# Optimization experiments

Measured on AMD Instinct MI355X. Metric: run time of the kernel, lower is better.

## Reference

```python
import jax, jax.numpy as jnp
import numpy as np

B, T, H, L, NB, NL = 32, 512, 256, 2048, 256, 4
F0_MIN, F0_MAX = 0.0, 1.0
E_MIN, E_MAX = 0.0, 1.0


def setup_inputs() -> dict:
    key = jax.random.key(0)
    ks = jax.random.split(key, 12)
    s = 1.0 / np.sqrt(H)
    return {
        "x": jax.random.normal(ks[0], (B, T, H), jnp.float32),
        "src_seq": jax.random.uniform(ks[1], (B, T, 3), jnp.float32, 1.0, 8.0),
        "duration_target": jax.random.randint(ks[2], (B, T), 0, 7, jnp.int32),
        "pitch_target": jax.random.uniform(ks[3], (B, L), jnp.float32),
        "energy_target": jax.random.uniform(ks[4], (B, L), jnp.float32),
        "src_mask": jnp.zeros((B, T), bool),
        "max_len": L,
        "dur_W": jax.random.normal(ks[5], (NL, H, H), jnp.float32) * s,
        "dur_b": jnp.zeros((NL, H), jnp.float32),
        "dur_w": jax.random.normal(ks[6], (H,), jnp.float32) * s,
        "dur_b2": jnp.zeros((1,), jnp.float32),
        "pit_W": jax.random.normal(ks[7], (NL, H, H), jnp.float32) * s,
        "pit_b": jnp.zeros((NL, H), jnp.float32),
        "pit_w": jax.random.normal(ks[8], (H,), jnp.float32) * s,
        "pit_b2": jnp.zeros((1,), jnp.float32),
        "en_W": jax.random.normal(ks[9], (NL, H, H), jnp.float32) * s,
        "en_b": jnp.zeros((NL, H), jnp.float32),
        "en_w": jax.random.normal(ks[10], (H,), jnp.float32) * s,
        "en_b2": jnp.zeros((1,), jnp.float32),
        "pitch_emb": jax.random.normal(ks[11], (2 * NB, H), jnp.float32),
        "energy_emb": jax.random.normal(jax.random.fold_in(key, 99), (2 * NB, H), jnp.float32),
    }


def _predictor(h, W, b, w, b2, mask):
    # stand-in for Decoder(n_layers=4) + Linear(H, 1) head
    for i in range(NL):
        h = jax.nn.relu(jnp.einsum('blh,hk->blk', h, W[i]) + b[i])
    out = jnp.einsum('blh,h->bl', h, w) + b2[0]
    return jnp.where(mask, 0.0, out)


def _length_regulate(x, dur, max_len):
    # cumsum-based repeat_interleave: frame m maps to token searchsorted(cumsum(dur), m, 'right')
    cum = jnp.cumsum(dur, axis=1)                      # [B, T]
    mel_len = jnp.minimum(cum[:, -1], max_len)         # [B]
    frames = jnp.arange(max_len)                       # [L]
    idx = jax.vmap(lambda c: jnp.searchsorted(c, frames, side='right'))(cum)
    idx = jnp.clip(idx, 0, x.shape[1] - 1)             # [B, L]
    out = jnp.take_along_axis(x, idx[:, :, None], axis=1)  # [B, L, H]
    mel_mask = frames[None, :] >= mel_len[:, None]     # True = padding
    out = out * (~mel_mask)[:, :, None]
    return out, mel_len, mel_mask


def reference(x, src_seq, duration_target, pitch_target, energy_target, src_mask, max_len,
              dur_W, dur_b, dur_w, dur_b2, pit_W, pit_b, pit_w, pit_b2,
              en_W, en_b, en_w, en_b2, pitch_emb, energy_emb):
    # duration predictor: LengthPredictor = decoder + linear + tanh, scaled by note lengths
    d = _predictor(x, dur_W, dur_b, dur_w, dur_b2, src_mask)
    log_duration_prediction = (jnp.tanh(d) + 1.0) * src_seq[:, :, 2]

    # length regulator (training path: duration_target provided)
    xe, mel_len, mel_mask = _length_regulate(x, duration_target, max_len)

    pitch_prediction = jax.nn.relu(_predictor(xe, pit_W, pit_b, pit_w, pit_b2, mel_mask))
    p_idx = jnp.ceil((pitch_target - F0_MIN) / (F0_MAX - F0_MIN) * NB).astype(jnp.int32)
    p_emb = pitch_emb[p_idx]                            # [B, L, H]

    energy_prediction = _predictor(xe, en_W, en_b, en_w, en_b2, mel_mask)
    e_idx = jnp.ceil((energy_target - E_MIN) / (E_MAX - E_MIN) * NB).astype(jnp.int32)
    e_emb = energy_emb[e_idx]                           # [B, L, H]

    out = xe + p_emb + e_emb
    return out, log_duration_prediction, pitch_prediction, energy_prediction, mel_len, mel_mask
```

## Files before the change

kernel.cpp:

```cpp
#include <hip/hip_runtime.h>

typedef _Float16 half_t;
typedef _Float16 half8 __attribute__((ext_vector_type(8)));
typedef float floatx4 __attribute__((ext_vector_type(4)));

#define HST 264
#define B_ 32
#define T_ 512
#define H_ 256
#define L_ 2048

__global__ void prep_weights_kernel(const float* __restrict__ dur_W,
                                    const float* __restrict__ pit_W,
                                    const float* __restrict__ en_W,
                                    half_t* __restrict__ Wp) {
  int g = blockIdx.x * 256 + threadIdx.x;
  int lane = g & 63;
  int t = g >> 6;
  int nt = t & 15;
  int kk = (t >> 4) & 7;
  int layer = (t >> 7) & 3;
  int pred = t >> 9;
  const float* W = (pred == 0 ? dur_W : (pred == 1 ? pit_W : en_W)) + layer * 65536;
  int n = nt * 16 + (lane & 15);
  int k0 = kk * 32 + (lane >> 4) * 8;
  half8 o;
#pragma unroll
  for (int j = 0; j < 8; ++j) o[j] = (half_t)W[(k0 + j) * 256 + n];
  *(half8*)&Wp[(size_t)t * 512 + lane * 8] = o;
}

__global__ void regulate_kernel(const float* __restrict__ x,
                                const int* __restrict__ dur,
                                const float* __restrict__ pitch_t,
                                const float* __restrict__ energy_t,
                                const float* __restrict__ pemb,
                                const float* __restrict__ eemb,
                                int* __restrict__ idx_ws,
                                int* __restrict__ ml_ws,
                                float* __restrict__ out0,
                                float* __restrict__ out4,
                                float* __restrict__ out5) {
  __shared__ int cum_l[T_];
  __shared__ int idx_l[128];
  __shared__ int ml_s;
  int tid = threadIdx.x;
  int b = blockIdx.x >> 4;
  int chunk = blockIdx.x & 15;

  if (tid < 64) {
    int l = tid;
    const int* dr = dur + b * T_;
    int v[8];
    int base = l * 8;
#pragma unroll
    for (int j = 0; j < 8; ++j) v[j] = dr[base + j];
#pragma unroll
    for (int j = 1; j < 8; ++j) v[j] += v[j - 1];
    int tot = v[7];
    int inc = tot;
    for (int d = 1; d < 64; d <<= 1) {
      int t = __shfl_up(inc, d);
      if (l >= d) inc += t;
    }
    int excl = inc - tot;
#pragma unroll
    for (int j = 0; j < 8; ++j) cum_l[base + j] = excl + v[j];
    if (l == 63) {
      int mel = min(inc, L_);
      ml_s = mel;
      if (chunk == 0) {
        ml_ws[b] = mel;
        out4[b] = (float)mel;
      }
    }
  }
  __syncthreads();
  int ml = ml_s;
  if (tid < 128) {
    int m = chunk * 128 + tid;
    int lo = 0;
#pragma unroll
    for (int sh = 8; sh >= 0; --sh) {
      int c = lo + (1 << sh);
      if (c <= T_ && cum_l[c - 1] <= m) lo = c;
    }
    int idx = min(lo, T_ - 1);
    idx_l[tid] = idx;
    int g = b * L_ + m;
    idx_ws[g] = idx;
    out5[g] = (m >= ml) ? 1.0f : 0.0f;
  }
  __syncthreads();
  int wv = tid >> 6, lane = tid & 63;
  for (int it = 0; it < 32; ++it) {
    int p = wv * 32 + it;
    int m = chunk * 128 + p;
    int g = b * L_ + m;
    int ir = idx_l[p];
    float xv0 = 0.f, xv1 = 0.f, xv2 = 0.f, xv3 = 0.f;
    if (m < ml) {
      const float4 xv = *(const float4*)&x[((size_t)(b * T_ + ir)) * H_ + lane * 4];
      xv0 = xv.x; xv1 = xv.y; xv2 = xv.z; xv3 = xv.w;
    }
    int pi = (int)ceilf(pitch_t[g] * 256.0f);
    int ei = (int)ceilf(energy_t[g] * 256.0f);
    const float4 pv = *(const float4*)&pemb[(size_t)pi * H_ + lane * 4];
    const float4 ev = *(const float4*)&eemb[(size_t)ei * H_ + lane * 4];
    float4 o;
    o.x = xv0 + pv.x + ev.x;
    o.y = xv1 + pv.y + ev.y;
    o.z = xv2 + pv.z + ev.z;
    o.w = xv3 + pv.w + ev.w;
    *(float4*)&out0[(size_t)g * H_ + lane * 4] = o;
  }
}

__global__ __launch_bounds__(256, 2) void predictor_kernel(
    const float* __restrict__ x,
    const half_t* __restrict__ Wp,
    const float* __restrict__ dur_b, const float* __restrict__ dur_w, const float* __restrict__ dur_b2,
    const float* __restrict__ pit_b, const float* __restrict__ pit_w, const float* __restrict__ pit_b2,
    const float* __restrict__ en_b,  const float* __restrict__ en_w,  const float* __restrict__ en_b2,
    const int* __restrict__ idx_ws, const int* __restrict__ mlw,
    const float* __restrict__ src_seq, const unsigned char* __restrict__ src_mask,
    float* __restrict__ out1, float* __restrict__ out2, float* __restrict__ out3) {
  __shared__ half_t hlds[128 * HST];
  int bid = blockIdx.x;
  int mode, blk;
  const half_t* W; const float* bias; const float* wh; const float* b2p; float* outp;
  if (bid < 512)       { mode = 1; blk = bid;        W = Wp + 262144; bias = pit_b; wh = pit_w; b2p = pit_b2; outp = out2; }
  else if (bid < 1024) { mode = 2; blk = bid - 512;  W = Wp + 524288; bias = en_b;  wh = en_w;  b2p = en_b2;  outp = out3; }
  else                 { mode = 0; blk = bid - 1024; W = Wp;          bias = dur_b; wh = dur_w; b2p = dur_b2; outp = out1; }

  int tid = threadIdx.x;
  int wv = tid >> 6, lane = tid & 63;
  int mi = lane & 15, qi = lane >> 4;
  int wrow0 = wv * 32;
  int brow0 = blk * 128;

  if (mode == 0) {
    for (int it = 0; it < 32; ++it) {
      int row = brow0 + wrow0 + it;
      const float4 xv = *(const float4*)&x[(size_t)row * H_ + lane * 4];
      half_t* dst = &hlds[(wrow0 + it) * HST + lane * 4];
      dst[0] = (half_t)xv.x; dst[1] = (half_t)xv.y;
      dst[2] = (half_t)xv.z; dst[3] = (half_t)xv.w;
    }
  } else {
    int b = brow0 >> 11;
    int m0 = brow0 & (L_ - 1);
    int ml = mlw[b];
    for (int it = 0; it < 32; ++it) {
      int m = m0 + wrow0 + it;
      float x0 = 0.f, x1 = 0.f, x2 = 0.f, x3 = 0.f;
      if (m < ml) {
        int ir = idx_ws[b * L_ + m];
        const float4 xv = *(const float4*)&x[((size_t)(b * T_ + ir)) * H_ + lane * 4];
        x0 = xv.x; x1 = xv.y; x2 = xv.z; x3 = xv.w;
      }
      half_t* dst = &hlds[(wrow0 + it) * HST + lane * 4];
      dst[0] = (half_t)x0; dst[1] = (half_t)x1;
      dst[2] = (half_t)x2; dst[3] = (half_t)x3;
    }
  }

  for (int layer = 0; layer < 4; ++layer) {
    half8 afr0[8], afr1[8];
#pragma unroll
    for (int kk = 0; kk < 8; ++kk) {
      afr0[kk] = *(const half8*)&hlds[(wrow0 + mi) * HST + kk * 32 + qi * 8];
      afr1[kk] = *(const half8*)&hlds[(wrow0 + 16 + mi) * HST + kk * 32 + qi * 8];
    }
    const half_t* wl = W + (size_t)layer * 65536;
    const float* bl = bias + layer * 256;
    half8 bA[8], bB[8];
#pragma unroll
    for (int kk = 0; kk < 8; ++kk)
      bA[kk] = *(const half8*)&wl[(size_t)(kk * 16 + 0) * 512 + lane * 8];
#pragma unroll 1
    for (int nt2 = 0; nt2 < 8; ++nt2) {
      int nt0 = nt2 * 2;
#pragma unroll
      for (int kk = 0; kk < 8; ++kk)
        bB[kk] = *(const half8*)&wl[(size_t)(kk * 16 + nt0 + 1) * 512 + lane * 8];
      {
        float bn = bl[nt0 * 16 + mi];
        floatx4 acc0 = {bn, bn, bn, bn};
        floatx4 acc1 = {bn, bn, bn, bn};
#pragma unroll
        for (int kk = 0; kk < 8; ++kk) {
          acc0 = __builtin_amdgcn_mfma_f32_16x16x32_f16(afr0[kk], bA[kk], acc0, 0, 0, 0);
          acc1 = __builtin_amdgcn_mfma_f32_16x16x32_f16(afr1[kk], bA[kk], acc1, 0, 0, 0);
        }
#pragma unroll
        for (int r = 0; r < 4; ++r) {
          float v0 = fmaxf(acc0[r], 0.f);
          float v1 = fmaxf(acc1[r], 0.f);
          hlds[(wrow0 + qi * 4 + r) * HST + nt0 * 16 + mi] = (half_t)v0;
          hlds[(wrow0 + 16 + qi * 4 + r) * HST + nt0 * 16 + mi] = (half_t)v1;
        }
      }
      if (nt2 < 7) {
#pragma unroll
        for (int kk = 0; kk < 8; ++kk)
          bA[kk] = *(const half8*)&wl[(size_t)(kk * 16 + nt0 + 2) * 512 + lane * 8];
      }
      {
        float bn = bl[(nt0 + 1) * 16 + mi];
        floatx4 acc0 = {bn, bn, bn, bn};
        floatx4 acc1 = {bn, bn, bn, bn};
#pragma unroll
        for (int kk = 0; kk < 8; ++kk) {
          acc0 = __builtin_amdgcn_mfma_f32_16x16x32_f16(afr0[kk], bB[kk], acc0, 0, 0, 0);
          acc1 = __builtin_amdgcn_mfma_f32_16x16x32_f16(afr1[kk], bB[kk], acc1, 0, 0, 0);
        }
#pragma unroll
        for (int r = 0; r < 4; ++r) {
          float v0 = fmaxf(acc0[r], 0.f);
          float v1 = fmaxf(acc1[r], 0.f);
          hlds[(wrow0 + qi * 4 + r) * HST + (nt0 + 1) * 16 + mi] = (half_t)v0;
          hlds[(wrow0 + 16 + qi * 4 + r) * HST + (nt0 + 1) * 16 + mi] = (half_t)v1;
        }
      }
    }
  }

  {
    int r = lane >> 1, hf = lane & 1;
    int lrow = wrow0 + r;
    float sum = 0.f;
    const half_t* hrow = &hlds[lrow * HST + hf * 128];
    const float* whp = wh + hf * 128;
#pragma unroll
    for (int j = 0; j < 16; ++j) {
      half8 hv = *(const half8*)&hrow[j * 8];
#pragma unroll
      for (int u = 0; u < 8; ++u) sum += (float)hv[u] * whp[j * 8 + u];
    }
    sum += __shfl_xor(sum, 1);
    if (hf == 0) {
      int row = brow0 + lrow;
      float d = sum + b2p[0];
      if (mode == 0) {
        if (src_mask[row]) d = 0.f;
        float s2 = src_seq[(size_t)row * 3 + 2];
        outp[row] = (tanhf(d) + 1.0f) * s2;
      } else {
        int b = row >> 11;
        int m = row & (L_ - 1);
        float v = (m >= mlw[b]) ? 0.f : d;
        outp[row] = (mode == 1) ? fmaxf(v, 0.f) : v;
      }
    }
  }
}

extern "C" void kernel_launch(void* const* d_in, const int* in_sizes, int n_in,
                              void* d_out, int out_size, void* d_ws, size_t ws_size,
                              hipStream_t stream) {
  const float* x        = (const float*)d_in[0];
  const float* src_seq  = (const float*)d_in[1];
  const int*   durt     = (const int*)d_in[2];
  const float* pitcht   = (const float*)d_in[3];
  const float* energyt  = (const float*)d_in[4];
  const unsigned char* src_mask = (const unsigned char*)d_in[5];
  const float* dur_W  = (const float*)d_in[7];
  const float* dur_b  = (const float*)d_in[8];
  const float* dur_w  = (const float*)d_in[9];
  const float* dur_b2 = (const float*)d_in[10];
  const float* pit_W  = (const float*)d_in[11];
  const float* pit_b  = (const float*)d_in[12];
  const float* pit_w  = (const float*)d_in[13];
  const float* pit_b2 = (const float*)d_in[14];
  const float* en_W   = (const float*)d_in[15];
  const float* en_b   = (const float*)d_in[16];
  const float* en_w   = (const float*)d_in[17];
  const float* en_b2  = (const float*)d_in[18];
  const float* pemb   = (const float*)d_in[19];
  const float* eemb   = (const float*)d_in[20];

  float* out0 = (float*)d_out;
  float* out1 = out0 + 16777216;
  float* out2 = out1 + 16384;
  float* out3 = out2 + 65536;
  float* out4 = out3 + 65536;
  float* out5 = out4 + 32;

  int* idx_ws = (int*)d_ws;
  int* ml_ws  = idx_ws + 65536;
  half_t* Wp  = (half_t*)((char*)d_ws + 262272);

  prep_weights_kernel<<<dim3(384), dim3(256), 0, stream>>>(dur_W, pit_W, en_W, Wp);
  regulate_kernel<<<dim3(512), dim3(256), 0, stream>>>(x, durt, pitcht, energyt, pemb, eemb,
                                                       idx_ws, ml_ws, out0, out4, out5);
  predictor_kernel<<<dim3(1152), dim3(256), 0, stream>>>(
      x, Wp,
      dur_b, dur_w, dur_b2,
      pit_b, pit_w, pit_b2,
      en_b, en_w, en_b2,
      idx_ws, ml_ws, src_seq, src_mask,
      out1, out2, out3);
}
```

Measured before the change: 282.7 us.

## Split regulate into meta and out0 kernels; restructure predictor to 2-wave column-split MFMA

```diff
diff --git a/kernel.cpp b/kernel.cpp
--- a/kernel.cpp
+++ b/kernel.cpp
@@ -1,6 +1,7 @@
 #include <hip/hip_runtime.h>
 
 typedef _Float16 half_t;
+typedef _Float16 half4 __attribute__((ext_vector_type(4)));
 typedef _Float16 half8 __attribute__((ext_vector_type(8)));
 typedef float floatx4 __attribute__((ext_vector_type(4)));
 
@@ -30,24 +31,19 @@
   *(half8*)&Wp[(size_t)t * 512 + lane * 8] = o;
 }
 
-__global__ void regulate_kernel(const float* __restrict__ x,
-                                const int* __restrict__ dur,
-                                const float* __restrict__ pitch_t,
-                                const float* __restrict__ energy_t,
-                                const float* __restrict__ pemb,
-                                const float* __restrict__ eemb,
-                                int* __restrict__ idx_ws,
-                                int* __restrict__ ml_ws,
-                                float* __restrict__ out0,
-                                float* __restrict__ out4,
-                                float* __restrict__ out5) {
+__global__ void meta_kernel(const int* __restrict__ dur,
+                            const float* __restrict__ pitch_t,
+                            const float* __restrict__ energy_t,
+                            int* __restrict__ idx_ws,
+                            int* __restrict__ pi_ws,
+                            int* __restrict__ ei_ws,
+                            int* __restrict__ ml_ws,
+                            float* __restrict__ out4,
+                            float* __restrict__ out5) {
   __shared__ int cum_l[T_];
-  __shared__ int idx_l[128];
   __shared__ int ml_s;
+  int b = blockIdx.x;
   int tid = threadIdx.x;
-  int b = blockIdx.x >> 4;
-  int chunk = blockIdx.x & 15;
-
   if (tid < 64) {
     int l = tid;
     const int* dr = dur + b * T_;
@@ -69,16 +65,15 @@
     if (l == 63) {
       int mel = min(inc, L_);
       ml_s = mel;
-      if (chunk == 0) {
-        ml_ws[b] = mel;
-        out4[b] = (float)mel;
-      }
+      ml_ws[b] = mel;
+      out4[b] = (float)mel;
     }
   }
   __syncthreads();
   int ml = ml_s;
-  if (tid < 128) {
-    int m = chunk * 128 + tid;
+#pragma unroll
+  for (int j = 0; j < 8; ++j) {
+    int m = j * 256 + tid;
     int lo = 0;
 #pragma unroll
     for (int sh = 8; sh >= 0; --sh) {
@@ -86,37 +81,43 @@
       if (c <= T_ && cum_l[c - 1] <= m) lo = c;
     }
     int idx = min(lo, T_ - 1);
-    idx_l[tid] = idx;
     int g = b * L_ + m;
     idx_ws[g] = idx;
+    pi_ws[g] = (int)ceilf(pitch_t[g] * 256.0f);
+    ei_ws[g] = (int)ceilf(energy_t[g] * 256.0f);
     out5[g] = (m >= ml) ? 1.0f : 0.0f;
   }
-  __syncthreads();
-  int wv = tid >> 6, lane = tid & 63;
-  for (int it = 0; it < 32; ++it) {
-    int p = wv * 32 + it;
-    int m = chunk * 128 + p;
-    int g = b * L_ + m;
-    int ir = idx_l[p];
-    float xv0 = 0.f, xv1 = 0.f, xv2 = 0.f, xv3 = 0.f;
-    if (m < ml) {
-      const float4 xv = *(const float4*)&x[((size_t)(b * T_ + ir)) * H_ + lane * 4];
-      xv0 = xv.x; xv1 = xv.y; xv2 = xv.z; xv3 = xv.w;
-    }
-    int pi = (int)ceilf(pitch_t[g] * 256.0f);
-    int ei = (int)ceilf(energy_t[g] * 256.0f);
-    const float4 pv = *(const float4*)&pemb[(size_t)pi * H_ + lane * 4];
-    const float4 ev = *(const float4*)&eemb[(size_t)ei * H_ + lane * 4];
-    float4 o;
-    o.x = xv0 + pv.x + ev.x;
-    o.y = xv1 + pv.y + ev.y;
-    o.z = xv2 + pv.z + ev.z;
-    o.w = xv3 + pv.w + ev.w;
-    *(float4*)&out0[(size_t)g * H_ + lane * 4] = o;
-  }
-}
-
-__global__ __launch_bounds__(256, 2) void predictor_kernel(
+}
+
+__global__ void out0_kernel(const float* __restrict__ x,
+                            const float* __restrict__ pemb,
+                            const float* __restrict__ eemb,
+                            const int* __restrict__ idx_ws,
+                            const int* __restrict__ pi_ws,
+                            const int* __restrict__ ei_ws,
+                            const int* __restrict__ ml_ws,
+                            float* __restrict__ out0) {
+  int wid = blockIdx.x * 4 + (threadIdx.x >> 6);
+  int lane = threadIdx.x & 63;
+  int b = wid >> 11;
+  int m = wid & (L_ - 1);
+  int ml = ml_ws[b];
+  int ir = idx_ws[wid];
+  int pi = pi_ws[wid];
+  int ei = ei_ws[wid];
+  float4 xv = {0.f, 0.f, 0.f, 0.f};
+  if (m < ml) xv = *(const float4*)&x[((size_t)(b * T_ + ir)) * H_ + lane * 4];
+  const float4 pv = *(const float4*)&pemb[(size_t)pi * H_ + lane * 4];
+  const float4 ev = *(const float4*)&eemb[(size_t)ei * H_ + lane * 4];
+  float4 o;
+  o.x = xv.x + pv.x + ev.x;
+  o.y = xv.y + pv.y + ev.y;
+  o.z = xv.z + pv.z + ev.z;
+  o.w = xv.w + pv.w + ev.w;
+  *(float4*)&out0[(size_t)wid * H_ + lane * 4] = o;
+}
+
+__global__ __launch_bounds__(128, 1) void predictor_kernel(
     const float* __restrict__ x,
     const half_t* __restrict__ Wp,
     const float* __restrict__ dur_b, const float* __restrict__ dur_w, const float* __restrict__ dur_b2,
@@ -136,122 +137,110 @@
   int tid = threadIdx.x;
   int wv = tid >> 6, lane = tid & 63;
   int mi = lane & 15, qi = lane >> 4;
-  int wrow0 = wv * 32;
   int brow0 = blk * 128;
 
   if (mode == 0) {
-    for (int it = 0; it < 32; ++it) {
-      int row = brow0 + wrow0 + it;
-      const float4 xv = *(const float4*)&x[(size_t)row * H_ + lane * 4];
-      half_t* dst = &hlds[(wrow0 + it) * HST + lane * 4];
-      dst[0] = (half_t)xv.x; dst[1] = (half_t)xv.y;
-      dst[2] = (half_t)xv.z; dst[3] = (half_t)xv.w;
+    for (int it = 0; it < 64; ++it) {
+      int rl = wv * 64 + it;
+      const float4 xv = *(const float4*)&x[(size_t)(brow0 + rl) * H_ + lane * 4];
+      half4 h4;
+      h4[0] = (half_t)xv.x; h4[1] = (half_t)xv.y;
+      h4[2] = (half_t)xv.z; h4[3] = (half_t)xv.w;
+      *(half4*)&hlds[rl * HST + lane * 4] = h4;
     }
   } else {
     int b = brow0 >> 11;
     int m0 = brow0 & (L_ - 1);
     int ml = mlw[b];
-    for (int it = 0; it < 32; ++it) {
-      int m = m0 + wrow0 + it;
-      float x0 = 0.f, x1 = 0.f, x2 = 0.f, x3 = 0.f;
+    for (int it = 0; it < 64; ++it) {
+      int rl = wv * 64 + it;
+      int m = m0 + rl;
+      float4 xv = {0.f, 0.f, 0.f, 0.f};
       if (m < ml) {
         int ir = idx_ws[b * L_ + m];
-        const float4 xv = *(const float4*)&x[((size_t)(b * T_ + ir)) * H_ + lane * 4];
-        x0 = xv.x; x1 = xv.y; x2 = xv.z; x3 = xv.w;
+        xv = *(const float4*)&x[((size_t)(b * T_ + ir)) * H_ + lane * 4];
       }
-      half_t* dst = &hlds[(wrow0 + it) * HST + lane * 4];
-      dst[0] = (half_t)x0; dst[1] = (half_t)x1;
-      dst[2] = (half_t)x2; dst[3] = (half_t)x3;
-    }
-  }
-
+      half4 h4;
+      h4[0] = (half_t)xv.x; h4[1] = (half_t)xv.y;
+      h4[2] = (half_t)xv.z; h4[3] = (half_t)xv.w;
+      *(half4*)&hlds[rl * HST + lane * 4] = h4;
+    }
+  }
+  __syncthreads();
+
+  int nt0 = wv * 8;
+#pragma unroll 1
   for (int layer = 0; layer < 4; ++layer) {
-    half8 afr0[8], afr1[8];
-#pragma unroll
-    for (int kk = 0; kk < 8; ++kk) {
-      afr0[kk] = *(const half8*)&hlds[(wrow0 + mi) * HST + kk * 32 + qi * 8];
-      afr1[kk] = *(const half8*)&hlds[(wrow0 + 16 + mi) * HST + kk * 32 + qi * 8];
-    }
+    half8 hf[8][8];
+#pragma unroll
+    for (int mt = 0; mt < 8; ++mt)
+#pragma unroll
+      for (int kk = 0; kk < 8; ++kk)
+        hf[mt][kk] = *(const half8*)&hlds[(mt * 16 + mi) * HST + kk * 32 + qi * 8];
+    __syncthreads();
+
     const half_t* wl = W + (size_t)layer * 65536;
     const float* bl = bias + layer * 256;
-    half8 bA[8], bB[8];
+    half8 wbuf[2][8];
+    float4 bbuf[2];
 #pragma unroll
     for (int kk = 0; kk < 8; ++kk)
-      bA[kk] = *(const half8*)&wl[(size_t)(kk * 16 + 0) * 512 + lane * 8];
-#pragma unroll 1
-    for (int nt2 = 0; nt2 < 8; ++nt2) {
-      int nt0 = nt2 * 2;
+      wbuf[0][kk] = *(const half8*)&wl[(size_t)(kk * 16 + nt0) * 512 + lane * 8];
+    bbuf[0] = *(const float4*)&bl[nt0 * 16 + qi * 4];
+
+#pragma unroll
+    for (int ntl = 0; ntl < 8; ++ntl) {
+      int cur = ntl & 1, nxt = cur ^ 1;
+      if (ntl < 7) {
+#pragma unroll
+        for (int kk = 0; kk < 8; ++kk)
+          wbuf[nxt][kk] = *(const half8*)&wl[(size_t)(kk * 16 + nt0 + ntl + 1) * 512 + lane * 8];
+        bbuf[nxt] = *(const float4*)&bl[(nt0 + ntl + 1) * 16 + qi * 4];
+      }
+      floatx4 acc[8];
+#pragma unroll
+      for (int mt = 0; mt < 8; ++mt)
+        acc[mt] = (floatx4){bbuf[cur].x, bbuf[cur].y, bbuf[cur].z, bbuf[cur].w};
 #pragma unroll
       for (int kk = 0; kk < 8; ++kk)
-        bB[kk] = *(const half8*)&wl[(size_t)(kk * 16 + nt0 + 1) * 512 + lane * 8];
-      {
-        float bn = bl[nt0 * 16 + mi];
-        floatx4 acc0 = {bn, bn, bn, bn};
-        floatx4 acc1 = {bn, bn, bn, bn};
-#pragma unroll
-        for (int kk = 0; kk < 8; ++kk) {
-          acc0 = __builtin_amdgcn_mfma_f32_16x16x32_f16(afr0[kk], bA[kk], acc0, 0, 0, 0);
-          acc1 = __builtin_amdgcn_mfma_f32_16x16x32_f16(afr1[kk], bA[kk], acc1, 0, 0, 0);
-        }
-#pragma unroll
-        for (int r = 0; r < 4; ++r) {
-          float v0 = fmaxf(acc0[r], 0.f);
-          float v1 = fmaxf(acc1[r], 0.f);
-          hlds[(wrow0 + qi * 4 + r) * HST + nt0 * 16 + mi] = (half_t)v0;
-          hlds[(wrow0 + 16 + qi * 4 + r) * HST + nt0 * 16 + mi] = (half_t)v1;
-        }
+#pragma unroll
+        for (int mt = 0; mt < 8; ++mt)
+          acc[mt] = __builtin_amdgcn_mfma_f32_16x16x32_f16(wbuf[cur][kk], hf[mt][kk], acc[mt], 0, 0, 0);
+      int colbase = (nt0 + ntl) * 16 + qi * 4;
+#pragma unroll
+      for (int mt = 0; mt < 8; ++mt) {
+        half4 h4;
+        h4[0] = (half_t)fmaxf(acc[mt][0], 0.f);
+        h4[1] = (half_t)fmaxf(acc[mt][1], 0.f);
+        h4[2] = (half_t)fmaxf(acc[mt][2], 0.f);
+        h4[3] = (half_t)fmaxf(acc[mt][3], 0.f);
+        *(half4*)&hlds[(mt * 16 + mi) * HST + colbase] = h4;
       }
-      if (nt2 < 7) {
-#pragma unroll
-        for (int kk = 0; kk < 8; ++kk)
-          bA[kk] = *(const half8*)&wl[(size_t)(kk * 16 + nt0 + 2) * 512 + lane * 8];
-      }
-      {
-        float bn = bl[(nt0 + 1) * 16 + mi];
-        floatx4 acc0 = {bn, bn, bn, bn};
-        floatx4 acc1 = {bn, bn, bn, bn};
-#pragma unroll
-        for (int kk = 0; kk < 8; ++kk) {
-          acc0 = __builtin_amdgcn_mfma_f32_16x16x32_f16(afr0[kk], bB[kk], acc0, 0, 0, 0);
-          acc1 = __builtin_amdgcn_mfma_f32_16x16x32_f16(afr1[kk], bB[kk], acc1, 0, 0, 0);
-        }
-#pragma unroll
-        for (int r = 0; r < 4; ++r) {
-          float v0 = fmaxf(acc0[r], 0.f);
-          float v1 = fmaxf(acc1[r], 0.f);
-          hlds[(wrow0 + qi * 4 + r) * HST + (nt0 + 1) * 16 + mi] = (half_t)v0;
-          hlds[(wrow0 + 16 + qi * 4 + r) * HST + (nt0 + 1) * 16 + mi] = (half_t)v1;
-        }
-      }
-    }
+    }
+    __syncthreads();
   }
 
   {
-    int r = lane >> 1, hf = lane & 1;
-    int lrow = wrow0 + r;
+    int rl = wv * 64 + lane;
     float sum = 0.f;
-    const half_t* hrow = &hlds[lrow * HST + hf * 128];
-    const float* whp = wh + hf * 128;
-#pragma unroll
-    for (int j = 0; j < 16; ++j) {
+    const half_t* hrow = &hlds[rl * HST];
+#pragma unroll
+    for (int j = 0; j < 32; ++j) {
       half8 hv = *(const half8*)&hrow[j * 8];
 #pragma unroll
-      for (int u = 0; u < 8; ++u) sum += (float)hv[u] * whp[j * 8 + u];
-    }
-    sum += __shfl_xor(sum, 1);
-    if (hf == 0) {
-      int row = brow0 + lrow;
-      float d = sum + b2p[0];
-      if (mode == 0) {
-        if (src_mask[row]) d = 0.f;
-        float s2 = src_seq[(size_t)row * 3 + 2];
-        outp[row] = (tanhf(d) + 1.0f) * s2;
-      } else {
-        int b = row >> 11;
-        int m = row & (L_ - 1);
-        float v = (m >= mlw[b]) ? 0.f : d;
-        outp[row] = (mode == 1) ? fmaxf(v, 0.f) : v;
-      }
+      for (int u = 0; u < 8; ++u) sum += (float)hv[u] * wh[j * 8 + u];
+    }
+    int row = brow0 + rl;
+    float d = sum + b2p[0];
+    if (mode == 0) {
+      if (src_mask[row]) d = 0.f;
+      float s2 = src_seq[(size_t)row * 3 + 2];
+      outp[row] = (tanhf(d) + 1.0f) * s2;
+    } else {
+      int b = row >> 11;
+      int m = row & (L_ - 1);
+      float v = (m >= mlw[b]) ? 0.f : d;
+      outp[row] = (mode == 1) ? fmaxf(v, 0.f) : v;
     }
   }
 }
@@ -288,13 +277,17 @@
   float* out5 = out4 + 32;
 
   int* idx_ws = (int*)d_ws;
-  int* ml_ws  = idx_ws + 65536;
-  half_t* Wp  = (half_t*)((char*)d_ws + 262272);
+  int* pi_ws  = idx_ws + 65536;
+  int* ei_ws  = pi_ws + 65536;
+  int* ml_ws  = ei_ws + 65536;
+  half_t* Wp  = (half_t*)((char*)d_ws + 786560);
 
   prep_weights_kernel<<<dim3(384), dim3(256), 0, stream>>>(dur_W, pit_W, en_W, Wp);
-  regulate_kernel<<<dim3(512), dim3(256), 0, stream>>>(x, durt, pitcht, energyt, pemb, eemb,
-                                                       idx_ws, ml_ws, out0, out4, out5);
-  predictor_kernel<<<dim3(1152), dim3(256), 0, stream>>>(
+  meta_kernel<<<dim3(32), dim3(256), 0, stream>>>(durt, pitcht, energyt,
+                                                  idx_ws, pi_ws, ei_ws, ml_ws, out4, out5);
+  out0_kernel<<<dim3(16384), dim3(256), 0, stream>>>(x, pemb, eemb,
+                                                     idx_ws, pi_ws, ei_ws, ml_ws, out0);
+  predictor_kernel<<<dim3(1152), dim3(128), 0, stream>>>(
       x, Wp,
       dur_b, dur_w, dur_b2,
       pit_b, pit_w, pit_b2,
```

New measurement: 275.3 us. 2.6% less time.
